# Optimization experiments

Measured on AMD Instinct MI355X. Metric: run time of the kernel, lower is better.

## Reference

```python
import jax, jax.numpy as jnp
import numpy as np

B = 2
DIMS = ((41, 800, 800), (21, 400, 400), (11, 200, 200), (6, 100, 100))  # (D,H,W)=(z,y,x) per level
VS = ((0.1, 0.1, 0.2), (0.2, 0.2, 0.4), (0.4, 0.4, 0.8), (0.8, 0.8, 1.6))  # (vx,vy,vz)
OFFSET = (0.0, -40.0, -3.0)  # world offset (x,y,z)
BN_EPS = 1e-3

OFFS27 = jnp.array([[z, y, x] for z in (-1, 0, 1) for y in (-1, 0, 1) for x in (-1, 0, 1)], jnp.int32)

# ---------------- numpy-side input construction ----------------

def _np_downsample(coords, out_dims):
    # active output sites of SparseConv3d(k=3, s=2, p=1): in = 2*o - 1 + kd, kd in 0..2
    outs = []
    for kz in range(3):
        for ky in range(3):
            for kx in range(3):
                o = coords[:, 1:] + 1 - np.array([kz, ky, kx])
                ok = (o % 2 == 0).all(1)
                oc = o // 2
                ok &= (oc >= 0).all(1)
                ok &= (oc[:, 0] < out_dims[0]) & (oc[:, 1] < out_dims[1]) & (oc[:, 2] < out_dims[2])
                outs.append(np.concatenate([coords[ok, :1], oc[ok]], 1))
    return np.unique(np.concatenate(outs, 0), axis=0).astype(np.int32)


def _make_coords(rng):
    per_batch = []
    D0, H0, W0 = DIMS[0]
    for b in range(B):
        nc = 120
        centers = np.stack([rng.integers(3, D0 - 4, nc), rng.integers(5, H0 - 6, nc), rng.integers(5, W0 - 6, nc)], 1)
        offs = rng.integers(-3, 4, (nc, 40, 3))
        p = np.clip((centers[:, None, :] + offs).reshape(-1, 3), 0, np.array(DIMS[0]) - 1)
        p = np.unique(p, axis=0)  # sorted lexicographically == sorted by linear key
        per_batch.append(np.concatenate([np.full((len(p), 1), b), p], 1))
    return np.concatenate(per_batch, 0).astype(np.int32)


def setup_inputs():
    rng = np.random.default_rng(0)
    coords0 = _make_coords(rng)
    coords1 = _np_downsample(coords0, DIMS[1])
    coords2 = _np_downsample(coords1, DIMS[2])
    coords3 = _np_downsample(coords2, DIMS[3])
    n = coords0.shape[0]
    c = coords0.astype(np.float64)
    x = OFFSET[0] + (c[:, 3] + 0.5) * VS[0][0] + rng.uniform(-0.04, 0.04, n)
    y = OFFSET[1] + (c[:, 2] + 0.5) * VS[0][1] + rng.uniform(-0.04, 0.04, n)
    z = OFFSET[2] + (c[:, 1] + 0.5) * VS[0][2] + rng.uniform(-0.08, 0.08, n)
    vf = np.stack([x, y, z, rng.uniform(0.0, 1.0, n)], 1).astype(np.float32)

    def conv_w(k, cin, cout):
        return (rng.standard_normal((k, cin, cout)) / np.sqrt(k * cin)).astype(np.float32)

    def bn_p(ch):
        return np.stack([1.0 + 0.05 * rng.standard_normal(ch), 0.05 * rng.standard_normal(ch)], 0).astype(np.float32)

    inp = dict(voxel_features=vf, coords0=coords0, coords1=coords1, coords2=coords2, coords3=coords3,
               w00=conv_w(27, 4, 16), b00=bn_p(16), w01=conv_w(27, 16, 16), b01=bn_p(16),
               wd0=conv_w(27, 16, 32), bd0=bn_p(32),
               w10=conv_w(27, 32, 32), b10=bn_p(32), w11=conv_w(27, 32, 32), b11=bn_p(32),
               wd1=conv_w(27, 32, 64), bd1=bn_p(64),
               w20=conv_w(27, 64, 64), b20=bn_p(64), w21=conv_w(27, 64, 64), b21=bn_p(64), w22=conv_w(27, 64, 64), b22=bn_p(64),
               wd2=conv_w(27, 64, 64), bd2=bn_p(64),
               w30=conv_w(27, 64, 64), b30=bn_p(64), w31=conv_w(27, 64, 64), b31=bn_p(64), w32=conv_w(27, 64, 64), b32=bn_p(64),
               we=(rng.standard_normal((64, 64)) / 8.0).astype(np.float32), be=bn_p(64),
               fc_w=(rng.standard_normal((64, 160)) / np.sqrt(160.0)).astype(np.float32),
               cls_w=(rng.standard_normal((1, 64)) / 8.0).astype(np.float32),
               reg_w=(rng.standard_normal((3, 64)) / 8.0).astype(np.float32))
    return {k: jnp.asarray(v) for k, v in inp.items()}

# ---------------- jax sparse-conv primitives ----------------

def _key(c, dims):
    D, H, W = dims
    return ((c[:, 0] * D + c[:, 1]) * H + c[:, 2]) * W + c[:, 3]


def _gather(nb_b, nb, feats, keys_sorted, dims):
    # nb: (N,27,3) candidate (z,y,x); gather rows of feats via sorted-key lookup, zeros if absent
    D, H, W = dims
    inb = (nb[..., 0] >= 0) & (nb[..., 0] < D) & (nb[..., 1] >= 0) & (nb[..., 1] < H) & (nb[..., 2] >= 0) & (nb[..., 2] < W)
    nbc = jnp.clip(nb, 0, jnp.array(dims, jnp.int32) - 1)
    qk = ((nb_b * D + nbc[..., 0]) * H + nbc[..., 1]) * W + nbc[..., 2]
    pos = jnp.clip(jnp.searchsorted(keys_sorted, qk), 0, keys_sorted.shape[0] - 1)
    found = inb & (keys_sorted[pos] == qk)
    return jnp.where(found[..., None], feats[pos], 0.0)


def _subm(feats, coords, keys, dims, w):
    nb = coords[:, None, 1:] + OFFS27[None]
    g = _gather(coords[:, None, 0], nb, feats, keys, dims)  # (N,27,Cin)
    return jnp.einsum('nkc,kco->no', g, w)


def _stride(feats, in_keys, in_dims, coords_out, w):
    nb = coords_out[:, None, 1:] * 2 + OFFS27[None]  # in = 2*o - 1 + kd
    g = _gather(coords_out[:, None, 0], nb, feats, in_keys, in_dims)
    return jnp.einsum('nkc,kco->no', g, w)


def _bn_relu(x, p):
    # train-mode BatchNorm1d over active voxels (biased var), eps=1e-3
    m = x.mean(0)
    v = jnp.mean((x - m) ** 2, 0)
    return jax.nn.relu((x - m) * jax.lax.rsqrt(v + BN_EPS) * p[0] + p[1])


def _t2p(coords, vs):
    c = coords.astype(jnp.float32)
    x = OFFSET[0] + (c[:, 3] + 0.5) * vs[0]
    y = OFFSET[1] + (c[:, 2] + 0.5) * vs[1]
    z = OFFSET[2] + (c[:, 1] + 0.5) * vs[2]
    return jnp.stack([c[:, 0], x, y, z], 1)


def _nn_interp(unknown, known, feats):
    # three_nn (squared L2, batch-separated, non-differentiable) + three_interpolate
    d2 = jnp.sum((unknown[:, None, 1:] - known[None, :, 1:]) ** 2, -1)
    d2 = d2 + 1e10 * (unknown[:, None, 0] != known[None, :, 0])
    d2 = jax.lax.stop_gradient(d2)
    negd, idx = jax.lax.top_k(-d2, 3)
    w = 1.0 / (-negd + 1e-8)
    w = w / w.sum(1, keepdims=True)
    return jnp.sum(feats[idx] * w[..., None], 1)


def _forward(voxel_features, w00, b00, w01, b01, wd0, bd0, w10, b10, w11, b11, wd1, bd1,
             w20, b20, w21, b21, w22, b22, wd2, bd2, w30, b30, w31, b31, w32, b32,
             we, be, fc_w, cls_w, reg_w, coords0, coords1, coords2, coords3):
    k0, k1 = _key(coords0, DIMS[0]), _key(coords1, DIMS[1])
    k2 = _key(coords2, DIMS[2])
    points_mean = jnp.concatenate([coords0[:, :1].astype(jnp.float32), voxel_features[:, :3]], 1)
    f = _bn_relu(_subm(voxel_features, coords0, k0, DIMS[0], w00), b00)
    f = _bn_relu(_subm(f, coords0, k0, DIMS[0], w01), b01)
    f = _bn_relu(_stride(f, k0, DIMS[0], coords1, wd0), bd0)
    f = _bn_relu(_subm(f, coords1, k1, DIMS[1], w10), b10)
    f = _bn_relu(_subm(f, coords1, k1, DIMS[1], w11), b11)
    p1 = _nn_interp(points_mean, _t2p(coords1, VS[1]), f)
    f = _bn_relu(_stride(f, k1, DIMS[1], coords2, wd1), bd1)
    f = _bn_relu(_subm(f, coords2, k2, DIMS[2], w20), b20)
    f = _bn_relu(_subm(f, coords2, k2, DIMS[2], w21), b21)
    f = _bn_relu(_subm(f, coords2, k2, DIMS[2], w22), b22)
    p2 = _nn_interp(points_mean, _t2p(coords2, VS[2]), f)
    f = _bn_relu(_stride(f, k2, DIMS[2], coords3, wd2), bd2)
    k3 = _key(coords3, DIMS[3])
    f = _bn_relu(_subm(f, coords3, k3, DIMS[3], w30), b30)
    f = _bn_relu(_subm(f, coords3, k3, DIMS[3], w31), b31)
    f = _bn_relu(_subm(f, coords3, k3, DIMS[3], w32), b32)
    p3 = _nn_interp(points_mean, _t2p(coords3, VS[3]), f)
    out = _bn_relu(f @ we, be)  # extra_conv: 1x1x1 SparseConv3d
    D3, H3, W3 = DIMS[3]
    dense = jnp.zeros((B, D3, H3, W3, 64), out.dtype).at[coords3[:, 0], coords3[:, 1], coords3[:, 2], coords3[:, 3]].set(out)
    xd = dense.transpose(0, 4, 1, 2, 3).reshape(B, 64 * D3, H3, W3)  # (N, C*D, H, W)
    pw = jnp.concatenate([p1, p2, p3], 1) @ fc_w.T
    return (xd, points_mean, pw @ cls_w.T, pw @ reg_w.T)


def reference(voxel_features, w00, b00, w01, b01, wd0, bd0, w10, b10, w11, b11, wd1, bd1,
              w20, b20, w21, b21, w22, b22, wd2, bd2, w30, b30, w31, b31, w32, b32,
              we, be, fc_w, cls_w, reg_w, coords0, coords1, coords2, coords3):
    return _forward(voxel_features, w00, b00, w01, b01, wd0, bd0, w10, b10, w11, b11, wd1, bd1,
                    w20, b20, w21, b21, w22, b22, wd2, bd2, w30, b30, w31, b31, w32, b32,
                    we, be, fc_w, cls_w, reg_w, coords0, coords1, coords2, coords3)
```

## Files before the change

### kernel.cpp

```cpp
#include <hip/hip_runtime.h>

#define OFFX 0.0f
#define OFFY -40.0f
#define OFFZ -3.0f
#define BNEPS 1e-3f
#define NCH 128
#define NG 9

typedef _Float16 h2_t __attribute__((ext_vector_type(2)));
__device__ inline h2_t u2h(unsigned u) { union { unsigned u; h2_t h; } x; x.u = u; return x.h; }
__device__ inline unsigned h2u(h2_t h) { union { unsigned u; h2_t h; } x; x.h = h; return x.u; }

__global__ void keys_k(const int* __restrict__ coords, int n, int D, int H, int W,
                       int* __restrict__ keys) {
  int i = blockIdx.x * 256 + threadIdx.x;
  if (i < n) {
    const int* c = coords + (size_t)i * 4;
    keys[i] = ((c[0] * D + c[1]) * H + c[2]) * W + c[3];
  }
}

__global__ void nbr_k(const int* __restrict__ coords, int np, const int* __restrict__ keys, int nk,
                      int D, int H, int W, int scale, int* __restrict__ nbr) {
  int t = blockIdx.x * 256 + threadIdx.x;
  if (t >= np * 27) return;
  int p = t / 27, k = t % 27;
  int kz = k / 9 - 1, ky = (k / 3) % 3 - 1, kx = k % 3 - 1;
  const int* c = coords + (size_t)p * 4;
  int z = c[1] * scale + kz, y = c[2] * scale + ky, x = c[3] * scale + kx;
  int r = -1;
  if (z >= 0 && z < D && y >= 0 && y < H && x >= 0 && x < W) {
    int q = ((c[0] * D + z) * H + y) * W + x;
    int lo = 0, hi = nk;
    while (lo < hi) { int m = (lo + hi) >> 1; if (keys[m] < q) lo = m + 1; else hi = m; }
    if (lo < nk && keys[lo] == q) r = lo;
  }
  nbr[t] = r;
}

struct WPrep { const float* src; unsigned* dst; int cin; int cout; };
struct WP13 { WPrep l[13]; };
__global__ void wprep_k(WP13 a) {
  WPrep w = a.l[blockIdx.y];
  int cp2 = w.cin / 2;
  int tot = 27 * cp2 * w.cout;
  int i = blockIdx.x * 256 + threadIdx.x;
  if (i >= tot) return;
  int o = i % w.cout, rest = i / w.cout;
  int cp = rest % cp2, k = rest / cp2;
  float lo = w.src[((size_t)k * w.cin + 2 * cp) * w.cout + o];
  float hi = w.src[((size_t)k * w.cin + 2 * cp + 1) * w.cout + o];
  h2_t h; h[0] = (_Float16)lo; h[1] = (_Float16)hi;
  w.dst[i] = h2u(h);
}

template<int CIN, int COUT>
__global__ __launch_bounds__(128) void convg_k(const float* __restrict__ feats,
                                               const int* __restrict__ nbr,
                                               const float* __restrict__ w, int n,
                                               float* __restrict__ partial, int gstride) {
  constexpr int TP = 32;
  constexpr int LDP = 36;
  constexpr int CO = COUT / 16;
  __shared__ float G[CIN * LDP];
  int tid = threadIdx.x;
  int pg = tid >> 4, cg = tid & 15;
  int p0 = blockIdx.x * TP;
  int k0 = blockIdx.y * 3;
  float acc[4][CO];
#pragma unroll
  for (int i = 0; i < 4; i++)
#pragma unroll
    for (int j = 0; j < CO; j++) acc[i][j] = 0.f;

  for (int kk = 0; kk < 3; kk++) {
    int k = k0 + kk;
    __syncthreads();
    for (int ch = tid; ch < TP * CIN / 4; ch += 128) {
      int r = ch & (TP - 1), c4 = ch / TP;
      int p = p0 + r;
      int idx = (p < n) ? nbr[(size_t)p * 27 + k] : -1;
      float4 fv = make_float4(0.f, 0.f, 0.f, 0.f);
      if (idx >= 0) fv = *(const float4*)(feats + (size_t)idx * CIN + c4 * 4);
      G[(c4 * 4 + 0) * LDP + r] = fv.x;
      G[(c4 * 4 + 1) * LDP + r] = fv.y;
      G[(c4 * 4 + 2) * LDP + r] = fv.z;
      G[(c4 * 4 + 3) * LDP + r] = fv.w;
    }
    __syncthreads();
    const float* wk = w + (size_t)k * CIN * COUT + cg * CO;
#pragma unroll
    for (int c = 0; c < CIN; c++) {
      float4 g4 = *(const float4*)&G[c * LDP + pg * 4];
      float wv[CO];
      if constexpr (CO == 4)      *(float4*)wv = *(const float4*)(wk + c * COUT);
      else if constexpr (CO == 2) *(float2*)wv = *(const float2*)(wk + c * COUT);
      else                        wv[0] = wk[c * COUT];
      float gp[4] = {g4.x, g4.y, g4.z, g4.w};
#pragma unroll
      for (int i = 0; i < 4; i++)
#pragma unroll
        for (int j = 0; j < CO; j++) acc[i][j] = fmaf(gp[i], wv[j], acc[i][j]);
    }
  }
#pragma unroll
  for (int i = 0; i < 4; i++) {
    int p = p0 + pg * 4 + i;
    if (p < n) {
      float* dst = partial + (size_t)blockIdx.y * gstride + (size_t)p * COUT + cg * CO;
      if constexpr (CO == 4)      *(float4*)dst = *(float4*)acc[i];
      else if constexpr (CO == 2) *(float2*)dst = *(float2*)acc[i];
      else                        dst[0] = acc[i][0];
    }
  }
}

template<int CIN, int COUT>
__global__ __launch_bounds__(128) void convh_k(const unsigned* __restrict__ fh,
                                               const int* __restrict__ nbr,
                                               const unsigned* __restrict__ wh, int n,
                                               float* __restrict__ partial, int gstride,
                                               const float* __restrict__ scsh) {
  constexpr int TP = 32;
  constexpr int LDPH = 36;
  constexpr int CO = COUT / 16;
  constexpr int CP = CIN / 2;
  __shared__ unsigned H[CP * LDPH];
  int tid = threadIdx.x;
  int pg = tid >> 4, cg = tid & 15;
  int p0 = blockIdx.x * TP;
  int k0 = blockIdx.y * 3;
  int r = tid & 31;
  int p = p0 + r;
  float acc[4][CO];
#pragma unroll
  for (int i = 0; i < 4; i++)
#pragma unroll
    for (int j = 0; j < CO; j++) acc[i][j] = 0.f;

  for (int kk = 0; kk < 3; kk++) {
    int k = k0 + kk;
    int idx = (p < n) ? nbr[(size_t)p * 27 + k] : -1;
    bool ok = idx >= 0;
    __syncthreads();
    if constexpr (CIN >= 32) {
      constexpr int NLD = CIN / 32;
#pragma unroll
      for (int it = 0; it < NLD; it++) {
        int q = (tid >> 5) + it * 4;
        uint4 u = make_uint4(0, 0, 0, 0);
        if (ok) u = *(const uint4*)(fh + (size_t)idx * CP + q * 4);
        unsigned uu[4] = {u.x, u.y, u.z, u.w};
#pragma unroll
        for (int j = 0; j < 4; j++) {
          int cp = q * 4 + j;
          unsigned outw = 0;
          if (ok) {
            h2_t h = u2h(uu[j]);
            float lo = fmaxf(fmaf((float)h[0], scsh[2 * cp], scsh[CIN + 2 * cp]), 0.f);
            float hi = fmaxf(fmaf((float)h[1], scsh[2 * cp + 1], scsh[CIN + 2 * cp + 1]), 0.f);
            h2_t o; o[0] = (_Float16)lo; o[1] = (_Float16)hi;
            outw = h2u(o);
          }
          H[cp * LDPH + r] = outw;
        }
      }
    } else {
      int q = tid >> 5;
      uint2 u = make_uint2(0, 0);
      if (ok) u = *(const uint2*)(fh + (size_t)idx * CP + q * 2);
      unsigned uu[2] = {u.x, u.y};
#pragma unroll
      for (int j = 0; j < 2; j++) {
        int cp = q * 2 + j;
        unsigned outw = 0;
        if (ok) {
          h2_t h = u2h(uu[j]);
          float lo = fmaxf(fmaf((float)h[0], scsh[2 * cp], scsh[CIN + 2 * cp]), 0.f);
          float hi = fmaxf(fmaf((float)h[1], scsh[2 * cp + 1], scsh[CIN + 2 * cp + 1]), 0.f);
          h2_t o; o[0] = (_Float16)lo; o[1] = (_Float16)hi;
          outw = h2u(o);
        }
        H[cp * LDPH + r] = outw;
      }
    }
    __syncthreads();
    const unsigned* wk = wh + (size_t)k * CP * COUT + cg * CO;
#pragma unroll 8
    for (int cp = 0; cp < CP; cp++) {
      uint4 g4 = *(const uint4*)&H[cp * LDPH + pg * 4];
      unsigned gg[4] = {g4.x, g4.y, g4.z, g4.w};
      unsigned wv[CO];
      if constexpr (CO == 4)      *(uint4*)wv = *(const uint4*)(wk + cp * COUT);
      else if constexpr (CO == 2) *(uint2*)wv = *(const uint2*)(wk + cp * COUT);
      else                        wv[0] = wk[cp * COUT];
#pragma unroll
      for (int i = 0; i < 4; i++)
#pragma unroll
        for (int j = 0; j < CO; j++)
          acc[i][j] = __builtin_amdgcn_fdot2(u2h(gg[i]), u2h(wv[j]), acc[i][j], false);
    }
  }
#pragma unroll
  for (int i = 0; i < 4; i++) {
    int pp = p0 + pg * 4 + i;
    if (pp < n) {
      float* dst = partial + (size_t)blockIdx.y * gstride + (size_t)pp * COUT + cg * CO;
      if constexpr (CO == 4)      *(float4*)dst = *(float4*)acc[i];
      else if constexpr (CO == 2) *(float2*)dst = *(float2*)acc[i];
      else                        dst[0] = acc[i][0];
    }
  }
}

__global__ void bn_k(const float* __restrict__ partial, int G, int gstride, int n, int C,
                     float* __restrict__ pre, unsigned* __restrict__ preh,
                     float* __restrict__ stats, const float* __restrict__ bnp,
                     float* __restrict__ scsh, int* __restrict__ ctr) {
  __shared__ float l1e[256], l2e[256], l1o[256], l2o[256];
  __shared__ int lastf;
  int t = threadIdx.x;
  int total = n * C;
  float s1e = 0.f, s2e = 0.f, s1o = 0.f, s2o = 0.f;
  for (int i2 = (blockIdx.x * 256 + t) * 2; i2 < total; i2 += NCH * 512) {
    float v0 = 0.f, v1 = 0.f;
    for (int g = 0; g < G; g++) {
      float2 pv = *(const float2*)(partial + (size_t)g * gstride + i2);
      v0 += pv.x; v1 += pv.y;
    }
    if (pre) *(float2*)(pre + i2) = make_float2(v0, v1);
    h2_t h; h[0] = (_Float16)v0; h[1] = (_Float16)v1;
    preh[i2 >> 1] = h2u(h);
    s1e += v0; s2e += v0 * v0; s1o += v1; s2o += v1 * v1;
  }
  l1e[t] = s1e; l2e[t] = s2e; l1o[t] = s1o; l2o[t] = s2o;
  for (int s = 128; s >= C / 2; s >>= 1) {
    __syncthreads();
    if (t < s) {
      l1e[t] += l1e[t + s]; l2e[t] += l2e[t + s];
      l1o[t] += l1o[t + s]; l2o[t] += l2o[t + s];
    }
  }
  __syncthreads();
  if (t < C / 2) {
    stats[((size_t)blockIdx.x * C + 2 * t) * 2]     = l1e[t];
    stats[((size_t)blockIdx.x * C + 2 * t) * 2 + 1] = l2e[t];
    stats[((size_t)blockIdx.x * C + 2 * t + 1) * 2]     = l1o[t];
    stats[((size_t)blockIdx.x * C + 2 * t + 1) * 2 + 1] = l2o[t];
  }
  __threadfence();
  __syncthreads();
  if (t == 0) lastf = (atomicAdd(ctr, 1) == NCH - 1) ? 1 : 0;
  __syncthreads();
  if (lastf) {
    __threadfence();
    if (t < C) {
      float a1 = 0.f, a2 = 0.f;
      for (int ch = 0; ch < NCH; ch++) {
        a1 += stats[((size_t)ch * C + t) * 2];
        a2 += stats[((size_t)ch * C + t) * 2 + 1];
      }
      float m = a1 / n;
      float v = a2 / n - m * m;
      float sc = bnp[t] / sqrtf(v + BNEPS);
      scsh[t] = sc;
      scsh[C + t] = bnp[C + t] - m * sc;
    }
  }
}

__global__ void pm_k(const float* __restrict__ vf, const int* __restrict__ c0, int n0,
                     float* __restrict__ pm, float* __restrict__ out1) {
  int i = blockIdx.x * 256 + threadIdx.x;
  if (i >= n0) return;
  float b = (float)c0[(size_t)i * 4];
  float x = vf[(size_t)i * 4], y = vf[(size_t)i * 4 + 1], z = vf[(size_t)i * 4 + 2];
  pm[(size_t)i * 4] = b; pm[(size_t)i * 4 + 1] = x; pm[(size_t)i * 4 + 2] = y; pm[(size_t)i * 4 + 3] = z;
  out1[(size_t)i * 4] = b; out1[(size_t)i * 4 + 1] = x; out1[(size_t)i * 4 + 2] = y; out1[(size_t)i * 4 + 3] = z;
}

__global__ void knnprep_k(const int* __restrict__ coords, int nl, float vx, float vy, float vz,
                          float4* __restrict__ kp4, int* __restrict__ bs) {
  int i = blockIdx.x * 256 + threadIdx.x;
  if (i >= nl) return;
  const int* c = coords + (size_t)i * 4;
  kp4[i] = make_float4(OFFX + (c[3] + 0.5f) * vx,
                       OFFY + (c[2] + 0.5f) * vy,
                       OFFZ + (c[1] + 0.5f) * vz, (float)c[0]);
  if (c[0] == 0 && (i + 1 == nl || coords[(size_t)(i + 1) * 4] == 1)) bs[0] = i + 1;
}

__global__ __launch_bounds__(256) void knn_k(const float4* __restrict__ pm4, int n0,
                                             const float4* __restrict__ kp4, int nl,
                                             const int* __restrict__ bsp,
                                             float* __restrict__ wv, int* __restrict__ iv) {
  __shared__ __align__(16) float4 kp[256];
  __shared__ int bl[4], bh[4];
  int tid = threadIdx.x;
  int wave = tid >> 6, lane = tid & 63;
  int u = blockIdx.x * 4 + wave;
  bool valid = u < n0;
  float4 up = pm4[valid ? u : (n0 - 1)];
  int bs = bsp[0];
  int lo = (up.x == 0.f) ? 0 : bs;
  int hi = (up.x == 0.f) ? bs : nl;
  if (!valid) { lo = 0; hi = 0; }
  if (lane == 0) { bl[wave] = valid ? lo : 0x7fffffff; bh[wave] = valid ? hi : 0; }
  __syncthreads();
  int blo = min(min(bl[0], bl[1]), min(bl[2], bl[3]));
  int bhi = max(max(bh[0], bh[1]), max(bh[2], bh[3]));
  float ux = up.y, uy = up.z, uz = up.w;
  float d0 = 3e38f, d1 = 3e38f, d2 = 3e38f;
  int i0 = -1, i1 = -1, i2 = -1;
#define INS1(DD, GI) { \
    bool l0 = (DD) < d0, l1 = (DD) < d1, l2 = (DD) < d2; \
    i2 = l2 ? (l1 ? i1 : (GI)) : i2; \
    i1 = l1 ? (l0 ? i0 : (GI)) : i1; \
    i0 = l0 ? (GI) : i0; \
    float t1_ = __builtin_amdgcn_fmed3f(d0, d1, (DD)); \
    float t2_ = __builtin_amdgcn_fmed3f(d1, d2, (DD)); \
    d0 = fminf(d0, (DD)); d1 = t1_; d2 = t2_; }
#define DIST(Q) fmaf(ux - (Q).x, ux - (Q).x, fmaf(uy - (Q).y, uy - (Q).y, (uz - (Q).z) * (uz - (Q).z)))
  for (int cb = blo; cb < bhi; cb += 256) {
    int m = bhi - cb; if (m > 256) m = 256;
    __syncthreads();
    if (tid < m) kp[tid] = kp4[cb + tid];
    __syncthreads();
    if (cb + 256 <= lo || cb >= hi) continue;
    if (m == 256 && cb >= lo && cb + 256 <= hi) {
      float4 q0 = kp[lane], q1 = kp[lane + 64], q2 = kp[lane + 128], q3 = kp[lane + 192];
      float a0 = DIST(q0), a1 = DIST(q1), a2 = DIST(q2), a3 = DIST(q3);
      INS1(a0, cb + lane) INS1(a1, cb + lane + 64) INS1(a2, cb + lane + 128) INS1(a3, cb + lane + 192)
    } else {
#pragma unroll
      for (int j = 0; j < 4; j++) {
        int i = lane + 64 * j;
        int e = cb + i;
        if (i < m && e >= lo && e < hi) {
          float4 q = kp[i];
          float dd = DIST(q);
          INS1(dd, e)
        }
      }
    }
  }
#pragma unroll
  for (int off = 1; off < 64; off <<= 1) {
    float e0 = __shfl_xor(d0, off), e1 = __shfl_xor(d1, off), e2 = __shfl_xor(d2, off);
    int j0 = __shfl_xor(i0, off), j1 = __shfl_xor(i1, off), j2 = __shfl_xor(i2, off);
    INS1(e0, j0) INS1(e1, j1) INS1(e2, j2)
  }
#undef DIST
#undef INS1
  if (valid && lane == 0) {
    float w0 = 1.f / (d0 + 1e-8f), w1 = 1.f / (d1 + 1e-8f), w2 = 1.f / (d2 + 1e-8f);
    float s = w0 + w1 + w2;
    wv[(size_t)u * 3] = w0 / s; wv[(size_t)u * 3 + 1] = w1 / s; wv[(size_t)u * 3 + 2] = w2 / s;
    iv[(size_t)u * 3] = i0; iv[(size_t)u * 3 + 1] = i1; iv[(size_t)u * 3 + 2] = i2;
  }
}

__global__ void interp_k(const float* __restrict__ f, int C, const float* __restrict__ scsh,
                         const float* __restrict__ wv, const int* __restrict__ iv, int n0,
                         float* __restrict__ X, int xoff) {
  int t = blockIdx.x * 256 + threadIdx.x;
  if (t >= n0 * C) return;
  int u = t / C, c = t % C;
  float sc = scsh[c], sh = scsh[C + c];
  float a0 = fmaxf(fmaf(f[(size_t)iv[(size_t)u * 3]     * C + c], sc, sh), 0.f);
  float a1 = fmaxf(fmaf(f[(size_t)iv[(size_t)u * 3 + 1] * C + c], sc, sh), 0.f);
  float a2 = fmaxf(fmaf(f[(size_t)iv[(size_t)u * 3 + 2] * C + c], sc, sh), 0.f);
  X[(size_t)u * 160 + xoff + c] = wv[(size_t)u * 3] * a0 + wv[(size_t)u * 3 + 1] * a1
                                + wv[(size_t)u * 3 + 2] * a2;
}

__global__ __launch_bounds__(256) void conv1x1_k(const float* __restrict__ f,
                                                 const float* __restrict__ scsh,
                                                 const float* __restrict__ we, int n,
                                                 float* __restrict__ out) {
  __shared__ float rows[256];
  int t = threadIdx.x;
  int p = blockIdx.x * 4 + (t >> 6), c = t & 63;
  rows[t] = (p < n) ? fmaxf(fmaf(f[(size_t)p * 64 + c], scsh[c], scsh[64 + c]), 0.f) : 0.f;
  __syncthreads();
  if (p >= n) return;
  const float* fr = rows + (t >> 6) * 64;
  float a = 0.f;
#pragma unroll 16
  for (int ci = 0; ci < 64; ci++) a = fmaf(fr[ci], we[ci * 64 + c], a);
  out[(size_t)p * 64 + c] = a;
}

__global__ void scatter_k(const float* __restrict__ pre, const float* __restrict__ scsh,
                          const int* __restrict__ c3, int n3, float* __restrict__ out0) {
  int t = blockIdx.x * 256 + threadIdx.x;
  if (t >= n3 * 64) return;
  int p = t >> 6, c = t & 63;
  const int* cc = c3 + (size_t)p * 4;
  size_t o = ((((size_t)cc[0] * 64 + c) * 6 + cc[1]) * 100 + cc[2]) * 100 + cc[3];
  out0[o] = fmaxf(fmaf(pre[t], scsh[c], scsh[64 + c]), 0.f);
}

__global__ __launch_bounds__(256) void head_k(const float* __restrict__ X,
                                              const float* __restrict__ fcw,
                                              const float* __restrict__ clsw,
                                              const float* __restrict__ regw,
                                              int n0, float* __restrict__ outc,
                                              float* __restrict__ outr) {
  __shared__ float fl[64 * 161];
  int t = threadIdx.x;
  for (int i = t; i < 64 * 160; i += 256) {
    int r = i / 160, c = i % 160;
    fl[r * 161 + c] = fcw[i];
  }
  __syncthreads();
  int wave = t >> 6, lane = t & 63;
  int u = blockIdx.x * 4 + wave;
  if (u >= n0) return;
  const float* xr = X + (size_t)u * 160;
  const float* wr = fl + (size_t)lane * 161;
  float a = 0.f;
#pragma unroll 8
  for (int i = 0; i < 160; i++) a = fmaf(xr[i], wr[i], a);
  float c = a * clsw[lane];
  float r0 = a * regw[lane], r1 = a * regw[64 + lane], r2 = a * regw[128 + lane];
  for (int off = 32; off; off >>= 1) {
    c  += __shfl_down(c, off);
    r0 += __shfl_down(r0, off);
    r1 += __shfl_down(r1, off);
    r2 += __shfl_down(r2, off);
  }
  if (lane == 0) {
    outc[u] = c;
    outr[(size_t)u * 3] = r0; outr[(size_t)u * 3 + 1] = r1; outr[(size_t)u * 3 + 2] = r2;
  }
}

extern "C" void kernel_launch(void* const* d_in, const int* in_sizes, int n_in,
                              void* d_out, int out_size, void* d_ws, size_t ws_size,
                              hipStream_t stream) {
  const float* vf  = (const float*)d_in[0];
  const int* c0 = (const int*)d_in[1];
  const int* c1 = (const int*)d_in[2];
  const int* c2 = (const int*)d_in[3];
  const int* c3 = (const int*)d_in[4];
  const float* w00 = (const float*)d_in[5];  const float* b00 = (const float*)d_in[6];
  const float* w01 = (const float*)d_in[7];  const float* b01 = (const float*)d_in[8];
  const float* wd0 = (const float*)d_in[9];  const float* bd0 = (const float*)d_in[10];
  const float* w10 = (const float*)d_in[11]; const float* b10 = (const float*)d_in[12];
  const float* w11 = (const float*)d_in[13]; const float* b11 = (const float*)d_in[14];
  const float* wd1 = (const float*)d_in[15]; const float* bd1 = (const float*)d_in[16];
  const float* w20 = (const float*)d_in[17]; const float* b20 = (const float*)d_in[18];
  const float* w21 = (const float*)d_in[19]; const float* b21 = (const float*)d_in[20];
  const float* w22 = (const float*)d_in[21]; const float* b22 = (const float*)d_in[22];
  const float* wd2 = (const float*)d_in[23]; const float* bd2 = (const float*)d_in[24];
  const float* w30 = (const float*)d_in[25]; const float* b30 = (const float*)d_in[26];
  const float* w31 = (const float*)d_in[27]; const float* b31 = (const float*)d_in[28];
  const float* w32 = (const float*)d_in[29]; const float* b32 = (const float*)d_in[30];
  const float* we  = (const float*)d_in[31]; const float* be  = (const float*)d_in[32];
  const float* fcw = (const float*)d_in[33];
  const float* clsw = (const float*)d_in[34];
  const float* regw = (const float*)d_in[35];

  int N0 = in_sizes[1] / 4, N1 = in_sizes[2] / 4, N2 = in_sizes[3] / 4, N3 = in_sizes[4] / 4;
  int maxN = N0; if (N1 > maxN) maxN = N1; if (N2 > maxN) maxN = N2; if (N3 > maxN) maxN = N3;

  auto cdiv = [](int a, int b) { return (a + b - 1) / b; };
  char* p = (char*)d_ws;
  auto alloc = [&](size_t bytes) { char* r = p; p += (bytes + 255) & ~(size_t)255; return r; };

  int* keys0 = (int*)alloc((size_t)N0 * 4);
  int* keys1 = (int*)alloc((size_t)N1 * 4);
  int* keys2 = (int*)alloc((size_t)N2 * 4);
  int* keys3 = (int*)alloc((size_t)N3 * 4);
  int* nbr0  = (int*)alloc((size_t)N0 * 27 * 4);
  int* nbrs1 = (int*)alloc((size_t)N1 * 27 * 4);
  int* nbr1  = (int*)alloc((size_t)N1 * 27 * 4);
  int* nbrs2 = (int*)alloc((size_t)N2 * 27 * 4);
  int* nbr2  = (int*)alloc((size_t)N2 * 27 * 4);
  int* nbrs3 = (int*)alloc((size_t)N3 * 27 * 4);
  int* nbr3  = (int*)alloc((size_t)N3 * 27 * 4);
  float* FA = (float*)alloc((size_t)maxN * 64 * 4);
  float* FB = (float*)alloc((size_t)maxN * 64 * 4);
  float* FC = (float*)alloc((size_t)maxN * 64 * 4);
  unsigned* FAh = (unsigned*)alloc((size_t)maxN * 32 * 4);
  unsigned* FBh = (unsigned*)alloc((size_t)maxN * 32 * 4);
  float* stats = (float*)alloc((size_t)NCH * 64 * 2 * 4);
  float* SC = (float*)alloc((size_t)15 * 128 * 4);
  int* ctrs = (int*)alloc(16 * 4);
  float* wv = (float*)alloc((size_t)N0 * 3 * 4);
  int*   iv = (int*)alloc((size_t)N0 * 3 * 4);
  float* X  = (float*)alloc((size_t)N0 * 160 * 4);
  float* pmb = (float*)alloc((size_t)N0 * 4 * 4);
  float4* kp1 = (float4*)alloc((size_t)N1 * 16);
  float4* kp2 = (float4*)alloc((size_t)N2 * 16);
  float4* kp3 = (float4*)alloc((size_t)N3 * 16);
  int* bsA = (int*)alloc(32);
  unsigned* whbuf = (unsigned*)alloc((size_t)452736 * 4);

  float* out0 = (float*)d_out;
  float* out1 = out0 + 7680000;
  float* outc = out1 + (size_t)N0 * 4;
  float* outr = outc + N0;
  float* partial = out0;

  auto scsh = [&](int L) { return SC + (size_t)L * 128; };

  const float* wsrc[13] = {w01, wd0, w10, w11, wd1, w20, w21, w22, wd2, w30, w31, w32, nullptr};
  int wcin[13]  = {16, 16, 32, 32, 32, 64, 64, 64, 64, 64, 64, 64, 0};
  int wcout[13] = {16, 32, 32, 32, 64, 64, 64, 64, 64, 64, 64, 64, 0};
  unsigned* wdst[13];
  size_t woff = 0;
  WP13 wp{};
  int nw = 12;
  for (int i = 0; i < nw; i++) {
    wdst[i] = whbuf + woff;
    wp.l[i] = WPrep{wsrc[i], wdst[i], wcin[i], wcout[i]};
    woff += (size_t)27 * (wcin[i] / 2) * wcout[i];
  }
  for (int i = nw; i < 13; i++) wp.l[i] = WPrep{w01, wdst[0], 16, 16};

  hipMemsetAsync(ctrs, 0, 16 * 4, stream);
  wprep_k<<<dim3(216, nw), 256, 0, stream>>>(wp);
  keys_k<<<cdiv(N0, 256), 256, 0, stream>>>(c0, N0, 41, 800, 800, keys0);
  keys_k<<<cdiv(N1, 256), 256, 0, stream>>>(c1, N1, 21, 400, 400, keys1);
  keys_k<<<cdiv(N2, 256), 256, 0, stream>>>(c2, N2, 11, 200, 200, keys2);
  keys_k<<<cdiv(N3, 256), 256, 0, stream>>>(c3, N3, 6, 100, 100, keys3);
  nbr_k<<<cdiv(N0 * 27, 256), 256, 0, stream>>>(c0, N0, keys0, N0, 41, 800, 800, 1, nbr0);
  nbr_k<<<cdiv(N1 * 27, 256), 256, 0, stream>>>(c1, N1, keys0, N0, 41, 800, 800, 2, nbrs1);
  nbr_k<<<cdiv(N1 * 27, 256), 256, 0, stream>>>(c1, N1, keys1, N1, 21, 400, 400, 1, nbr1);
  nbr_k<<<cdiv(N2 * 27, 256), 256, 0, stream>>>(c2, N2, keys1, N1, 21, 400, 400, 2, nbrs2);
  nbr_k<<<cdiv(N2 * 27, 256), 256, 0, stream>>>(c2, N2, keys2, N2, 11, 200, 200, 1, nbr2);
  nbr_k<<<cdiv(N3 * 27, 256), 256, 0, stream>>>(c3, N3, keys2, N2, 11, 200, 200, 2, nbrs3);
  nbr_k<<<cdiv(N3 * 27, 256), 256, 0, stream>>>(c3, N3, keys3, N3, 6, 100, 100, 1, nbr3);
  pm_k<<<cdiv(N0, 256), 256, 0, stream>>>(vf, c0, N0, pmb, out1);
  knnprep_k<<<cdiv(N1, 256), 256, 0, stream>>>(c1, N1, 0.2f, 0.2f, 0.4f, kp1, bsA + 0);
  knnprep_k<<<cdiv(N2, 256), 256, 0, stream>>>(c2, N2, 0.4f, 0.4f, 0.8f, kp2, bsA + 1);
  knnprep_k<<<cdiv(N3, 256), 256, 0, stream>>>(c3, N3, 0.8f, 0.8f, 1.6f, kp3, bsA + 2);

  auto convh = [&](const unsigned* fhin, const int* nb, int wi, int n, int cin, int cout,
                   const float* ss) {
    dim3 g(cdiv(n, 32), NG);
    int gs = n * cout;
    const unsigned* wh = wdst[wi];
    if (cin == 16 && cout == 16)
      convh_k<16, 16><<<g, 128, 0, stream>>>(fhin, nb, wh, n, partial, gs, ss);
    else if (cin == 16 && cout == 32)
      convh_k<16, 32><<<g, 128, 0, stream>>>(fhin, nb, wh, n, partial, gs, ss);
    else if (cin == 32 && cout == 32)
      convh_k<32, 32><<<g, 128, 0, stream>>>(fhin, nb, wh, n, partial, gs, ss);
    else if (cin == 32 && cout == 64)
      convh_k<32, 64><<<g, 128, 0, stream>>>(fhin, nb, wh, n, partial, gs, ss);
    else
      convh_k<64, 64><<<g, 128, 0, stream>>>(fhin, nb, wh, n, partial, gs, ss);
  };
  auto bnp = [&](const float* bnpar, int n, int C, float* pre, unsigned* preh, int L) {
    bn_k<<<NCH, 256, 0, stream>>>(partial, NG, n * C, n, C, pre, preh, stats, bnpar,
                                  scsh(L), ctrs + L);
  };
  auto knn = [&](const float4* kp4, const int* bsl, int nl, const float* f, int C, int L,
                 int xoff) {
    knn_k<<<cdiv(N0, 4), 256, 0, stream>>>((const float4*)pmb, N0, kp4, nl, bsl, wv, iv);
    interp_k<<<cdiv(N0 * C, 256), 256, 0, stream>>>(f, C, scsh(L), wv, iv, N0, X, xoff);
  };

  convg_k<4, 16><<<dim3(cdiv(N0, 32), NG), 128, 0, stream>>>(vf, nbr0, w00, N0, partial, N0 * 16);
  bnp(b00, N0, 16, nullptr, FAh, 0);
  convh(FAh, nbr0, 0, N0, 16, 16, scsh(0));   bnp(b01, N0, 16, nullptr, FBh, 1);
  convh(FBh, nbrs1, 1, N1, 16, 32, scsh(1));  bnp(bd0, N1, 32, nullptr, FAh, 2);
  convh(FAh, nbr1, 2, N1, 32, 32, scsh(2));   bnp(b10, N1, 32, nullptr, FBh, 3);
  convh(FBh, nbr1, 3, N1, 32, 32, scsh(3));   bnp(b11, N1, 32, FA, FAh, 4);
  knn(kp1, bsA + 0, N1, FA, 32, 4, 0);
  convh(FAh, nbrs2, 4, N2, 32, 64, scsh(4));  bnp(bd1, N2, 64, nullptr, FBh, 5);
  convh(FBh, nbr2, 5, N2, 64, 64, scsh(5));   bnp(b20, N2, 64, nullptr, FAh, 6);
  convh(FAh, nbr2, 6, N2, 64, 64, scsh(6));   bnp(b21, N2, 64, nullptr, FBh, 7);
  convh(FBh, nbr2, 7, N2, 64, 64, scsh(7));   bnp(b22, N2, 64, FA, FAh, 8);
  knn(kp2, bsA + 1, N2, FA, 64, 8, 32);
  convh(FAh, nbrs3, 8, N3, 64, 64, scsh(8));  bnp(bd2, N3, 64, nullptr, FBh, 9);
  convh(FBh, nbr3, 9, N3, 64, 64, scsh(9));   bnp(b30, N3, 64, nullptr, FAh, 10);
  convh(FAh, nbr3, 10, N3, 64, 64, scsh(10)); bnp(b31, N3, 64, nullptr, FBh, 11);
  convh(FBh, nbr3, 11, N3, 64, 64, scsh(11)); bnp(b32, N3, 64, FA, FAh, 12);
  knn(kp3, bsA + 2, N3, FA, 64, 12, 96);

  conv1x1_k<<<cdiv(N3, 4), 256, 0, stream>>>(FA, scsh(12), we, N3, FC);
  bn_k<<<NCH, 256, 0, stream>>>(FC, 1, 0, N3, 64, FB, FBh, stats, be, scsh(13), ctrs + 13);
  hipMemsetAsync(d_out, 0, (size_t)7680000 * 4, stream);
  scatter_k<<<cdiv(N3 * 64, 256), 256, 0, stream>>>(FB, scsh(13), c3, N3, out0);
  head_k<<<cdiv(N0, 4), 256, 0, stream>>>(X, fcw, clsw, regw, N0, outc, outr);
}
```

Baseline: 923.5 us.

## Prefetch next neighbor gather in conv and read fp16 features downstream

The sparse conv kernel now loads all three neighbor indices up front and register-prefetches the next kernel offset's gathered feature row while the current one is being multiplied, so gather latency overlaps the dot-product loop. Separately, interp and the 1x1 conv now read the fp16 pre-activation buffer instead of a separate fp32 copy, so bn_k no longer writes the fp32 output at those stages. This adds register pressure, fully unrolls the inner loop for the CIN=16 path, and slightly lowers the precision of the interpolation and 1x1-conv inputs.

```diff
diff --git a/kernel.cpp b/kernel.cpp
--- a/kernel.cpp
+++ b/kernel.cpp
@@ -132,25 +132,37 @@
   int k0 = blockIdx.y * 3;
   int r = tid & 31;
   int p = p0 + r;
+  int sidx[3];
+  if (p < n) {
+    const int* nb = nbr + (size_t)p * 27 + k0;
+    sidx[0] = nb[0]; sidx[1] = nb[1]; sidx[2] = nb[2];
+  } else { sidx[0] = sidx[1] = sidx[2] = -1; }
+
   float acc[4][CO];
 #pragma unroll
   for (int i = 0; i < 4; i++)
 #pragma unroll
     for (int j = 0; j < CO; j++) acc[i][j] = 0.f;
 
-  for (int kk = 0; kk < 3; kk++) {
-    int k = k0 + kk;
-    int idx = (p < n) ? nbr[(size_t)p * 27 + k] : -1;
-    bool ok = idx >= 0;
-    __syncthreads();
-    if constexpr (CIN >= 32) {
-      constexpr int NLD = CIN / 32;
+  if constexpr (CIN >= 32) {
+    constexpr int NLD = CIN / 32;
+    uint4 pf[NLD];
+    {
+      int idx = sidx[0];
 #pragma unroll
       for (int it = 0; it < NLD; it++) {
         int q = (tid >> 5) + it * 4;
-        uint4 u = make_uint4(0, 0, 0, 0);
-        if (ok) u = *(const uint4*)(fh + (size_t)idx * CP + q * 4);
-        unsigned uu[4] = {u.x, u.y, u.z, u.w};
+        pf[it] = (idx >= 0) ? *(const uint4*)(fh + (size_t)idx * CP + q * 4)
+                            : make_uint4(0, 0, 0, 0);
+      }
+    }
+    for (int kk = 0; kk < 3; kk++) {
+      bool ok = sidx[kk] >= 0;
+      __syncthreads();
+#pragma unroll
+      for (int it = 0; it < NLD; it++) {
+        int q = (tid >> 5) + it * 4;
+        unsigned uu[4] = {pf[it].x, pf[it].y, pf[it].z, pf[it].w};
 #pragma unroll
         for (int j = 0; j < 4; j++) {
           int cp = q * 4 + j;
@@ -165,11 +177,43 @@
           H[cp * LDPH + r] = outw;
         }
       }
-    } else {
-      int q = tid >> 5;
-      uint2 u = make_uint2(0, 0);
-      if (ok) u = *(const uint2*)(fh + (size_t)idx * CP + q * 2);
-      unsigned uu[2] = {u.x, u.y};
+      if (kk < 2) {
+        int idx = sidx[kk + 1];
+#pragma unroll
+        for (int it = 0; it < NLD; it++) {
+          int q = (tid >> 5) + it * 4;
+          pf[it] = (idx >= 0) ? *(const uint4*)(fh + (size_t)idx * CP + q * 4)
+                              : make_uint4(0, 0, 0, 0);
+        }
+      }
+      __syncthreads();
+      const unsigned* wk = wh + (size_t)(k0 + kk) * CP * COUT + cg * CO;
+#pragma unroll 8
+      for (int cp = 0; cp < CP; cp++) {
+        uint4 g4 = *(const uint4*)&H[cp * LDPH + pg * 4];
+        unsigned gg[4] = {g4.x, g4.y, g4.z, g4.w};
+        unsigned wv[CO];
+        if constexpr (CO == 4)      *(uint4*)wv = *(const uint4*)(wk + cp * COUT);
+        else if constexpr (CO == 2) *(uint2*)wv = *(const uint2*)(wk + cp * COUT);
+        else                        wv[0] = wk[cp * COUT];
+#pragma unroll
+        for (int i = 0; i < 4; i++)
+#pragma unroll
+          for (int j = 0; j < CO; j++)
+            acc[i][j] = __builtin_amdgcn_fdot2(u2h(gg[i]), u2h(wv[j]), acc[i][j], false);
+      }
+    }
+  } else {
+    int q = tid >> 5;
+    uint2 pf2;
+    {
+      int idx = sidx[0];
+      pf2 = (idx >= 0) ? *(const uint2*)(fh + (size_t)idx * CP + q * 2) : make_uint2(0, 0);
+    }
+    for (int kk = 0; kk < 3; kk++) {
+      bool ok = sidx[kk] >= 0;
+      __syncthreads();
+      unsigned uu[2] = {pf2.x, pf2.y};
 #pragma unroll
       for (int j = 0; j < 2; j++) {
         int cp = q * 2 + j;
@@ -183,22 +227,26 @@
         }
         H[cp * LDPH + r] = outw;
       }
-    }
-    __syncthreads();
-    const unsigned* wk = wh + (size_t)k * CP * COUT + cg * CO;
-#pragma unroll 8
-    for (int cp = 0; cp < CP; cp++) {
-      uint4 g4 = *(const uint4*)&H[cp * LDPH + pg * 4];
-      unsigned gg[4] = {g4.x, g4.y, g4.z, g4.w};
-      unsigned wv[CO];
-      if constexpr (CO == 4)      *(uint4*)wv = *(const uint4*)(wk + cp * COUT);
-      else if constexpr (CO == 2) *(uint2*)wv = *(const uint2*)(wk + cp * COUT);
-      else                        wv[0] = wk[cp * COUT];
-#pragma unroll
-      for (int i = 0; i < 4; i++)
-#pragma unroll
-        for (int j = 0; j < CO; j++)
-          acc[i][j] = __builtin_amdgcn_fdot2(u2h(gg[i]), u2h(wv[j]), acc[i][j], false);
+      if (kk < 2) {
+        int idx = sidx[kk + 1];
+        pf2 = (idx >= 0) ? *(const uint2*)(fh + (size_t)idx * CP + q * 2) : make_uint2(0, 0);
+      }
+      __syncthreads();
+      const unsigned* wk = wh + (size_t)(k0 + kk) * CP * COUT + cg * CO;
+#pragma unroll
+      for (int cp = 0; cp < CP; cp++) {
+        uint4 g4 = *(const uint4*)&H[cp * LDPH + pg * 4];
+        unsigned gg[4] = {g4.x, g4.y, g4.z, g4.w};
+        unsigned wv[CO];
+        if constexpr (CO == 4)      *(uint4*)wv = *(const uint4*)(wk + cp * COUT);
+        else if constexpr (CO == 2) *(uint2*)wv = *(const uint2*)(wk + cp * COUT);
+        else                        wv[0] = wk[cp * COUT];
+#pragma unroll
+        for (int i = 0; i < 4; i++)
+#pragma unroll
+          for (int j = 0; j < CO; j++)
+            acc[i][j] = __builtin_amdgcn_fdot2(u2h(gg[i]), u2h(wv[j]), acc[i][j], false);
+      }
     }
   }
 #pragma unroll
@@ -360,28 +408,38 @@
   }
 }
 
-__global__ void interp_k(const float* __restrict__ f, int C, const float* __restrict__ scsh,
+__global__ void interp_k(const unsigned* __restrict__ fh, int C, const float* __restrict__ scsh,
                          const float* __restrict__ wv, const int* __restrict__ iv, int n0,
                          float* __restrict__ X, int xoff) {
   int t = blockIdx.x * 256 + threadIdx.x;
   if (t >= n0 * C) return;
   int u = t / C, c = t % C;
+  int cp = c >> 1, sel = c & 1;
+  int CP = C >> 1;
   float sc = scsh[c], sh = scsh[C + c];
-  float a0 = fmaxf(fmaf(f[(size_t)iv[(size_t)u * 3]     * C + c], sc, sh), 0.f);
-  float a1 = fmaxf(fmaf(f[(size_t)iv[(size_t)u * 3 + 1] * C + c], sc, sh), 0.f);
-  float a2 = fmaxf(fmaf(f[(size_t)iv[(size_t)u * 3 + 2] * C + c], sc, sh), 0.f);
+  h2_t h0 = u2h(fh[(size_t)iv[(size_t)u * 3]     * CP + cp]);
+  h2_t h1 = u2h(fh[(size_t)iv[(size_t)u * 3 + 1] * CP + cp]);
+  h2_t h2v = u2h(fh[(size_t)iv[(size_t)u * 3 + 2] * CP + cp]);
+  float a0 = fmaxf(fmaf((float)h0[sel], sc, sh), 0.f);
+  float a1 = fmaxf(fmaf((float)h1[sel], sc, sh), 0.f);
+  float a2 = fmaxf(fmaf((float)h2v[sel], sc, sh), 0.f);
   X[(size_t)u * 160 + xoff + c] = wv[(size_t)u * 3] * a0 + wv[(size_t)u * 3 + 1] * a1
                                 + wv[(size_t)u * 3 + 2] * a2;
 }
 
-__global__ __launch_bounds__(256) void conv1x1_k(const float* __restrict__ f,
+__global__ __launch_bounds__(256) void conv1x1_k(const unsigned* __restrict__ fh,
                                                  const float* __restrict__ scsh,
                                                  const float* __restrict__ we, int n,
                                                  float* __restrict__ out) {
   __shared__ float rows[256];
   int t = threadIdx.x;
   int p = blockIdx.x * 4 + (t >> 6), c = t & 63;
-  rows[t] = (p < n) ? fmaxf(fmaf(f[(size_t)p * 64 + c], scsh[c], scsh[64 + c]), 0.f) : 0.f;
+  float v = 0.f;
+  if (p < n) {
+    h2_t h = u2h(fh[(size_t)p * 32 + (c >> 1)]);
+    v = fmaxf(fmaf((float)h[c & 1], scsh[c], scsh[64 + c]), 0.f);
+  }
+  rows[t] = v;
   __syncthreads();
   if (p >= n) return;
   const float* fr = rows + (t >> 6) * 64;
@@ -558,10 +616,10 @@
     bn_k<<<NCH, 256, 0, stream>>>(partial, NG, n * C, n, C, pre, preh, stats, bnpar,
                                   scsh(L), ctrs + L);
   };
-  auto knn = [&](const float4* kp4, const int* bsl, int nl, const float* f, int C, int L,
+  auto knn = [&](const float4* kp4, const int* bsl, int nl, const unsigned* fh, int C, int L,
                  int xoff) {
     knn_k<<<cdiv(N0, 4), 256, 0, stream>>>((const float4*)pmb, N0, kp4, nl, bsl, wv, iv);
-    interp_k<<<cdiv(N0 * C, 256), 256, 0, stream>>>(f, C, scsh(L), wv, iv, N0, X, xoff);
+    interp_k<<<cdiv(N0 * C, 256), 256, 0, stream>>>(fh, C, scsh(L), wv, iv, N0, X, xoff);
   };
 
   convg_k<4, 16><<<dim3(cdiv(N0, 32), NG), 128, 0, stream>>>(vf, nbr0, w00, N0, partial, N0 * 16);
@@ -569,20 +627,20 @@
   convh(FAh, nbr0, 0, N0, 16, 16, scsh(0));   bnp(b01, N0, 16, nullptr, FBh, 1);
   convh(FBh, nbrs1, 1, N1, 16, 32, scsh(1));  bnp(bd0, N1, 32, nullptr, FAh, 2);
   convh(FAh, nbr1, 2, N1, 32, 32, scsh(2));   bnp(b10, N1, 32, nullptr, FBh, 3);
-  convh(FBh, nbr1, 3, N1, 32, 32, scsh(3));   bnp(b11, N1, 32, FA, FAh, 4);
-  knn(kp1, bsA + 0, N1, FA, 32, 4, 0);
+  convh(FBh, nbr1, 3, N1, 32, 32, scsh(3));   bnp(b11, N1, 32, nullptr, FAh, 4);
+  knn(kp1, bsA + 0, N1, FAh, 32, 4, 0);
   convh(FAh, nbrs2, 4, N2, 32, 64, scsh(4));  bnp(bd1, N2, 64, nullptr, FBh, 5);
   convh(FBh, nbr2, 5, N2, 64, 64, scsh(5));   bnp(b20, N2, 64, nullptr, FAh, 6);
   convh(FAh, nbr2, 6, N2, 64, 64, scsh(6));   bnp(b21, N2, 64, nullptr, FBh, 7);
-  convh(FBh, nbr2, 7, N2, 64, 64, scsh(7));   bnp(b22, N2, 64, FA, FAh, 8);
-  knn(kp2, bsA + 1, N2, FA, 64, 8, 32);
+  convh(FBh, nbr2, 7, N2, 64, 64, scsh(7));   bnp(b22, N2, 64, nullptr, FAh, 8);
+  knn(kp2, bsA + 1, N2, FAh, 64, 8, 32);
   convh(FAh, nbrs3, 8, N3, 64, 64, scsh(8));  bnp(bd2, N3, 64, nullptr, FBh, 9);
   convh(FBh, nbr3, 9, N3, 64, 64, scsh(9));   bnp(b30, N3, 64, nullptr, FAh, 10);
   convh(FAh, nbr3, 10, N3, 64, 64, scsh(10)); bnp(b31, N3, 64, nullptr, FBh, 11);
-  convh(FBh, nbr3, 11, N3, 64, 64, scsh(11)); bnp(b32, N3, 64, FA, FAh, 12);
-  knn(kp3, bsA + 2, N3, FA, 64, 12, 96);
-
-  conv1x1_k<<<cdiv(N3, 4), 256, 0, stream>>>(FA, scsh(12), we, N3, FC);
+  convh(FBh, nbr3, 11, N3, 64, 64, scsh(11)); bnp(b32, N3, 64, nullptr, FAh, 12);
+  knn(kp3, bsA + 2, N3, FAh, 64, 12, 96);
+
+  conv1x1_k<<<cdiv(N3, 4), 256, 0, stream>>>(FAh, scsh(12), we, N3, FC);
   bn_k<<<NCH, 256, 0, stream>>>(FC, 1, 0, N3, 64, FB, FBh, stats, be, scsh(13), ctrs + 13);
   hipMemsetAsync(d_out, 0, (size_t)7680000 * 4, stream);
   scatter_k<<<cdiv(N3 * 64, 256), 256, 0, stream>>>(FB, scsh(13), c3, N3, out0);
```

New measurement: 932.0 us. Within noise of the previous version (+0.9%).
